# Optimization experiments

Measured on AMD Instinct MI355X. Metric: run time of the kernel, lower is better.

Reference implementation:

```python
import jax, jax.numpy as jnp
import numpy as np

N, E, G = 50000, 800000, 64
IN, HID, H, OUT = 128, 64, 4, 10


def _gat_layer(x, src, dst, W, a_src, a_dst, b):
    # x: [N, Fin]; W: [H*C, Fin]; a_src/a_dst: [H, C]; b: [H*C]
    n = x.shape[0]
    C = a_src.shape[1]
    h = (x @ W.T).reshape(n, H, C)                      # [N, H, C]
    e_src = jnp.einsum('nhc,hc->nh', h, a_src)          # [N, H]
    e_dst = jnp.einsum('nhc,hc->nh', h, a_dst)          # [N, H]
    logits = jax.nn.leaky_relu(e_src[src] + e_dst[dst], 0.2)  # [E', H]
    # segment softmax over destination node
    m = jax.ops.segment_max(logits, dst, num_segments=n)
    ex = jnp.exp(logits - m[dst])
    denom = jax.ops.segment_sum(ex, dst, num_segments=n)
    alpha = ex / (denom[dst] + 1e-16)                   # [E', H]
    msg = h[src] * alpha[:, :, None]                    # [E', H, C]
    out = jax.ops.segment_sum(msg, dst, num_segments=n) # [N, H, C]
    return out.reshape(n, H * C) + b


def setup_inputs() -> dict:
    key = jax.random.key(0)
    ks = jax.random.split(key, 20)
    x = jax.random.normal(ks[0], (N, IN), dtype=jnp.float32)
    edge_index = jax.random.randint(ks[1], (2, E), 0, N, dtype=jnp.int64)
    batch = jnp.sort(jax.random.randint(ks[2], (N,), 0, G, dtype=jnp.int64))

    def glorot(k, shape):
        fan = shape[-1]
        return jax.random.normal(k, shape, dtype=jnp.float32) / jnp.sqrt(jnp.float32(fan))

    ins = [IN, HID * H, HID * H]
    params = {}
    for i, fin in enumerate(ins, start=1):
        params[f'W{i}'] = glorot(ks[3 * i], (H * HID, fin))
        params[f'a_src{i}'] = glorot(ks[3 * i + 1], (H, HID))
        params[f'a_dst{i}'] = glorot(ks[3 * i + 2], (H, HID))
        params[f'b{i}'] = jnp.zeros((H * HID,), dtype=jnp.float32)
    params['Wl'] = glorot(ks[13], (OUT, H * HID))
    params['bl'] = jnp.zeros((OUT,), dtype=jnp.float32)
    return dict(x=x, edge_index=edge_index, batch=batch, **params)


def reference(x, edge_index, batch,
              W1, a_src1, a_dst1, b1,
              W2, a_src2, a_dst2, b2,
              W3, a_src3, a_dst3, b3,
              Wl, bl):
    n = x.shape[0]
    loops = jnp.arange(n, dtype=edge_index.dtype)
    src = jnp.concatenate([edge_index[0], loops])  # add self-loops (PyG default)
    dst = jnp.concatenate([edge_index[1], loops])

    h = jax.nn.elu(_gat_layer(x, src, dst, W1, a_src1, a_dst1, b1))
    h = jax.nn.elu(_gat_layer(h, src, dst, W2, a_src2, a_dst2, b2))
    h = _gat_layer(h, src, dst, W3, a_src3, a_dst3, b3)

    # global mean pool over graphs
    sums = jax.ops.segment_sum(h, batch, num_segments=G)          # [G, H*HID]
    counts = jax.ops.segment_sum(jnp.ones((n,), h.dtype), batch, num_segments=G)
    pooled = sums / jnp.maximum(counts, 1.0)[:, None]
    return pooled @ Wl.T + bl                                      # [G, OUT]
```

## Files before the change

kernel.cpp:

```cpp
#include <hip/hip_runtime.h>
#include <hip/hip_bf16.h>
#include <math.h>

#define NNODES 50000
#define NEDGES 800000
#define NGRAPH 64
#define FIN 128
#define HC 256
#define NHEAD 4
#define NOUT 10
#define ETOT (NEDGES + NNODES)
#define NB196 ((NNODES + 255) / 256)
#define BUCKET_MAX 5376
#define S1CHUNK 4096
#define NBS1 ((ETOT + S1CHUNK - 1) / S1CHUNK)


typedef unsigned short u16;
typedef unsigned char u8;
typedef __attribute__((ext_vector_type(8))) short short8;
typedef __attribute__((ext_vector_type(4))) float f32x4;
typedef __attribute__((ext_vector_type(2))) float f32x2;

__device__ inline u16 f2b(float f) {
    union { float f; unsigned u; } v; v.f = f;
    unsigned r = v.u + 0x7FFF + ((v.u >> 16) & 1);
    return (u16)(r >> 16);
}
__device__ inline float b2f(u16 u) {
    union { unsigned u; float f; } v; v.u = ((unsigned)u) << 16; return v.f;
}

__device__ inline void gload_lds16(const void* g, void* l) {
    __builtin_amdgcn_global_load_lds(
        (const __attribute__((address_space(1))) unsigned*)g,
        (__attribute__((address_space(3))) unsigned*)l, 16, 0, 0);
}


#define CS0 (NNODES * FIN)
#define CS1 (HC * FIN)
#define CS2 (HC * HC)
#define NBCONV (((CS0 + CS1 + 2 * CS2) / 4 + 255) / 256)
#define NBDEG ((ETOT + 255) / 256)

__global__ void prep_kernel(const float* __restrict__ x, const float* __restrict__ W1,
                            const float* __restrict__ W2, const float* __restrict__ W3,
                            u16* __restrict__ xb, u16* __restrict__ w1b,
                            u16* __restrict__ w2b, u16* __restrict__ w3b,
                            const int* __restrict__ ei, int* __restrict__ deg) {
    int b = blockIdx.x;
    if (b < NBCONV) {
        long i = (long)(b * 256 + threadIdx.x) * 4;
        if (i < CS0) {
            float4 v = *(const float4*)(x + i);
            ushort4 o;
            o.x = f2b(v.x); o.y = f2b(v.y); o.z = f2b(v.z); o.w = f2b(v.w);
            *(ushort4*)(xb + i) = o;
        } else if (i < CS0 + CS1) {
            long off = i - CS0;
            float4 v = *(const float4*)(W1 + off);
            ushort4 o;
            o.x = f2b(v.x); o.y = f2b(v.y); o.z = f2b(v.z); o.w = f2b(v.w);
            *(ushort4*)(w1b + off) = o;
        } else if (i < CS0 + CS1 + 2 * CS2) {
            const float* src; u16* dst; long off;
            if (i < CS0 + CS1 + CS2) { src = W2; dst = w2b; off = i - CS0 - CS1; }
            else                     { src = W3; dst = w3b; off = i - CS0 - CS1 - CS2; }
            float4 v = *(const float4*)(src + off);
            int row = (int)(off >> 8), col = (int)(off & 255);
            float vv[4] = {v.x, v.y, v.z, v.w};
            #pragma unroll
            for (int k = 0; k < 4; ++k) {
                int c = col + k;
                int pp = (c & ~63) | ((c & 15) << 2) | ((c >> 4) & 3);
                dst[row * 256 + pp] = f2b(vv[k]);
            }
        }
    } else {
        int e = (b - NBCONV) * 256 + threadIdx.x;
        if (e >= ETOT) return;
        int dstn = (e < NEDGES) ? ei[NEDGES + e] : (e - NEDGES);
        atomicAdd(&deg[dstn], 1);
    }
}


__global__ __launch_bounds__(256) void scan1_kernel(const int* __restrict__ deg,
                                                    int* __restrict__ off,
                                                    int* __restrict__ bsum) {
    int tid = threadIdx.x, lane = tid & 63, wid = tid >> 6;
    int i = blockIdx.x * 256 + tid;
    __shared__ int ws[4];
    int v = (i < NNODES) ? deg[i] : 0;
    int x = v;
    #pragma unroll
    for (int o = 1; o < 64; o <<= 1) {
        int t = __shfl_up(x, o);
        if (lane >= o) x += t;
    }
    if (lane == 63) ws[wid] = x;
    __syncthreads();
    if (tid < 4) {
        int w = ws[tid];
        #pragma unroll
        for (int o = 1; o < 4; o <<= 1) {
            int t = __shfl_up(w, o, 4);
            if ((tid & 3) >= o) w += t;
        }
        ws[tid] = w;
    }
    __syncthreads();
    int wexcl = wid ? ws[wid - 1] : 0;
    if (i <= NNODES) off[i] = x - v + wexcl;
    if (tid == 0) bsum[blockIdx.x] = ws[3];
}

__global__ __launch_bounds__(256) void scan2_kernel(int* __restrict__ bsum,
                                                    const int* __restrict__ batch,
                                                    int* __restrict__ goff) {
    int tid = threadIdx.x, lane = tid & 63, wid = tid >> 6;
    __shared__ int ws[4];
    int v = (tid < NB196) ? bsum[tid] : 0;
    int x = v;
    #pragma unroll
    for (int o = 1; o < 64; o <<= 1) {
        int t = __shfl_up(x, o);
        if (lane >= o) x += t;
    }
    if (lane == 63) ws[wid] = x;
    __syncthreads();
    if (tid < 4) {
        int w = ws[tid];
        #pragma unroll
        for (int o = 1; o < 4; o <<= 1) {
            int t = __shfl_up(w, o, 4);
            if ((tid & 3) >= o) w += t;
        }
        ws[tid] = w;
    }
    __syncthreads();
    int wexcl = wid ? ws[wid - 1] : 0;
    if (tid <= NB196) bsum[tid] = x - v + wexcl;
    if (tid <= NGRAPH) {
        int g = tid, lo = 0, hi = NNODES;
        while (lo < hi) {
            int mid = (lo + hi) >> 1;
            if (batch[mid] < g) lo = mid + 1; else hi = mid;
        }
        goff[g] = lo;
    }
}


__global__ __launch_bounds__(256) void scatter1_kernel(const int* __restrict__ ei,
                                                       const int* __restrict__ bsum,
                                                       int* __restrict__ bcur,
                                                       unsigned* __restrict__ tmp) {
    __shared__ int hist[NB196];
    __shared__ int basec[NB196];
    int tid = threadIdx.x;
    int e0 = blockIdx.x * S1CHUNK;
    for (int i = tid; i < NB196; i += 256) hist[i] = 0;
    __syncthreads();
    int bkt[16], rnk[16];
    unsigned pk[16];
    #pragma unroll
    for (int k = 0; k < 16; ++k) {
        int e = e0 + k * 256 + tid;
        bkt[k] = -1;
        if (e < ETOT) {
            int src, dst;
            if (e < NEDGES) { src = ei[e]; dst = ei[NEDGES + e]; }
            else            { src = dst = e - NEDGES; }
            int b = dst >> 8;
            bkt[k] = b;
            rnk[k] = atomicAdd(&hist[b], 1);
            pk[k] = (unsigned)src | ((unsigned)(dst & 255) << 16);
        }
    }
    __syncthreads();
    for (int i = tid; i < NB196; i += 256) {
        int h = hist[i];
        basec[i] = h ? atomicAdd(&bcur[i], h) : 0;
    }
    __syncthreads();
    #pragma unroll
    for (int k = 0; k < 16; ++k) {
        if (bkt[k] >= 0)
            tmp[bsum[bkt[k]] + basec[bkt[k]] + rnk[k]] = pk[k];
    }
}

__global__ __launch_bounds__(256) void scatter2_kernel(const unsigned* __restrict__ tmp,
                                                       const int* __restrict__ off,
                                                       const int* __restrict__ bsum,
                                                       int* __restrict__ ssrc) {
    __shared__ int cnt[256];
    __shared__ int ldss[BUCKET_MAX];
    int b = blockIdx.x;
    int tid = threadIdx.x;
    int s = bsum[b], e2 = bsum[b + 1];
    int total = e2 - s;
    if (total > BUCKET_MAX) total = BUCKET_MAX;
    cnt[tid] = 0;
    __syncthreads();
    const int* offb = off + b * 256;
    for (int i = s + tid; i < e2; i += 256) {
        unsigned pk = tmp[i];
        int src = (int)(pk & 0xFFFFu);
        int ld = (int)(pk >> 16);
        int rank = atomicAdd(&cnt[ld], 1);
        int idx = offb[ld] + rank;
        if (idx < BUCKET_MAX) ldss[idx] = src;
    }
    __syncthreads();
    for (int i = tid; i < total; i += 256)
        ssrc[s + i] = ldss[i];
}


#define TBM 128
#define TBN 128
#define TBK 32

__global__ __launch_bounds__(256) void gemm_mfma(const u16* __restrict__ A,
                                                 const u16* __restrict__ B,
                                                 u8* __restrict__ C, int K,
                                                 const float* __restrict__ asrc,
                                                 const float* __restrict__ adst,
                                                 float* __restrict__ es,
                                                 float* __restrict__ ed) {
    __shared__ u16 Als[TBM * TBK];
    __shared__ u16 Bls[TBN * TBK];
    int tid = threadIdx.x;
    int wave = tid >> 6, lane = tid & 63;
    int brow = blockIdx.x * TBM, bcol = blockIdx.y * TBN;
    int m_base = (wave >> 1) * 64, n_base = (wave & 1) * 64;
    int r0 = tid >> 2, kc = (tid & 3) * 8;
    int lquad = lane >> 4, l16 = lane & 15;

    f32x4 acc[4][4] = {};

    const u16* ga0 = A + (size_t)(brow + r0) * K + kc;
    const u16* ga1 = A + (size_t)(brow + 64 + r0) * K + kc;
    const u16* gb0 = B + (size_t)(bcol + r0) * K + kc;
    const u16* gb1 = B + (size_t)(bcol + 64 + r0) * K + kc;
    u16* la0 = &Als[r0 * TBK + kc];
    u16* la1 = &Als[(64 + r0) * TBK + kc];
    u16* lb0 = &Bls[r0 * TBK + kc];
    u16* lb1 = &Bls[(64 + r0) * TBK + kc];

    for (int k0 = 0; k0 < K; k0 += TBK) {
        __syncthreads();
        gload_lds16(ga0 + k0, la0);
        gload_lds16(ga1 + k0, la1);
        gload_lds16(gb0 + k0, lb0);
        gload_lds16(gb1 + k0, lb1);
        __syncthreads();
        short8 fa[4], fb[4];
        #pragma unroll
        for (int i = 0; i < 4; ++i) {
            fa[i] = *(const short8*)(&Als[(m_base + i * 16 + l16) * TBK + lquad * 8]);
            fb[i] = *(const short8*)(&Bls[(n_base + i * 16 + l16) * TBK + lquad * 8]);
        }
        #pragma unroll
        for (int i = 0; i < 4; ++i)
            #pragma unroll
            for (int j = 0; j < 4; ++j)
                acc[i][j] = __builtin_amdgcn_mfma_f32_16x16x32_bf16(fa[i], fb[j], acc[i][j], 0, 0, 0);
    }

    #pragma unroll
    for (int i = 0; i < 4; ++i) {
        int rbase = brow + m_base + i * 16 + lquad * 4;
        #pragma unroll
        for (int r = 0; r < 4; ++r) {
            int row = rbase + r;
            if (row < NNODES) {
                int u = 0;
                u = __builtin_amdgcn_cvt_pk_fp8_f32(acc[i][0][r], acc[i][1][r], u, false);
                u = __builtin_amdgcn_cvt_pk_fp8_f32(acc[i][2][r], acc[i][3][r], u, true);
                *(int*)(C + (size_t)row * HC + bcol + n_base + l16 * 4) = u;
            }
        }
    }

    int head = (bcol + n_base) >> 6;
    float asv[4], adv[4];
    #pragma unroll
    for (int j = 0; j < 4; ++j) {
        asv[j] = asrc[head * 64 + j * 16 + l16];
        adv[j] = adst[head * 64 + j * 16 + l16];
    }
    #pragma unroll
    for (int i = 0; i < 4; ++i) {
        #pragma unroll
        for (int r = 0; r < 4; ++r) {
            float ps = 0.f, pd = 0.f;
            #pragma unroll
            for (int j = 0; j < 4; ++j) {
                ps = fmaf(acc[i][j][r], asv[j], ps);
                pd = fmaf(acc[i][j][r], adv[j], pd);
            }
            #pragma unroll
            for (int o = 1; o < 16; o <<= 1) {
                ps += __shfl_xor(ps, o);
                pd += __shfl_xor(pd, o);
            }
            int row = brow + m_base + i * 16 + lquad * 4 + r;
            if (l16 == 0 && row < NNODES) {
                es[row * 4 + head] = ps;
                ed[row * 4 + head] = pd;
            }
        }
    }
}


__global__ __launch_bounds__(256) void aggregate_kernel(const u8* __restrict__ h,
                                                        const int* __restrict__ ssrc,
                                                        const int* __restrict__ off,
                                                        const int* __restrict__ bsum,
                                                        const float* __restrict__ es,
                                                        const float* __restrict__ ed,
                                                        const float* __restrict__ bias,
                                                        u16* __restrict__ out,
                                                        int apply_elu) {
    __shared__ int2 xch[4][4][17];
    const unsigned* h32 = (const unsigned*)h;
    int wid = threadIdx.x >> 6;
    int dst = blockIdx.x * 4 + wid;
    if (dst >= NNODES) return;
    int lane = threadIdx.x & 63;
    int head = lane >> 4;
    int j16 = lane & 15;
    int s = off[dst] + bsum[dst >> 8];
    int e = off[dst + 1] + bsum[(dst + 1) >> 8];
    float edh = ed[dst * 4 + head];
    int2* myslot = &xch[wid][head][0];

    float a0 = 0.f, a1 = 0.f, a2 = 0.f, a3 = 0.f, dpriv = 0.f;

    int base = s;
    for (; base + 16 <= e; base += 16) {
        int mysrc = ssrc[base + j16];
        float l = es[mysrc * 4 + head] + edh;
        l = fmaxf(l, 0.2f * l);
        float myex = __expf(l);
        dpriv += myex;
        myslot[j16] = make_int2(mysrc, __float_as_int(myex));
        #pragma unroll
        for (int j = 0; j < 16; ++j) {
            int2 pr = myslot[j];
            float exj = __int_as_float(pr.y);
            unsigned hv = h32[(unsigned)pr.x * 64 + lane];
            f32x2 lo = __builtin_amdgcn_cvt_pk_f32_fp8(hv, false);
            f32x2 hi = __builtin_amdgcn_cvt_pk_f32_fp8(hv, true);
            a0 += lo.x * exj;
            a1 += lo.y * exj;
            a2 += hi.x * exj;
            a3 += hi.y * exj;
        }
    }
    int cnt = e - base;
    if (cnt > 0) {
        int mysrc = 0; float myex = 0.f;
        if (j16 < cnt) {
            mysrc = ssrc[base + j16];
            float l = es[mysrc * 4 + head] + edh;
            l = fmaxf(l, 0.2f * l);
            myex = __expf(l);
            dpriv += myex;
        }
        myslot[j16] = make_int2(mysrc, __float_as_int(myex));
        for (int j = 0; j < cnt; ++j) {
            int2 pr = myslot[j];
            float exj = __int_as_float(pr.y);
            unsigned hv = h32[(unsigned)pr.x * 64 + lane];
            f32x2 lo = __builtin_amdgcn_cvt_pk_f32_fp8(hv, false);
            f32x2 hi = __builtin_amdgcn_cvt_pk_f32_fp8(hv, true);
            a0 += lo.x * exj;
            a1 += lo.y * exj;
            a2 += hi.x * exj;
            a3 += hi.y * exj;
        }
    }
    #pragma unroll
    for (int o = 1; o < 16; o <<= 1) dpriv += __shfl_xor(dpriv, o);
    float inv = 1.f / (dpriv + 1e-16f);
    int bbase = ((lane >> 4) << 6) | (lane & 15);
    float b0 = bias[bbase], b1 = bias[bbase + 16], b2 = bias[bbase + 32], b3 = bias[bbase + 48];
    float o0 = a0 * inv + b0;
    float o1 = a1 * inv + b1;
    float o2 = a2 * inv + b2;
    float o3 = a3 * inv + b3;
    if (apply_elu) {
        o0 = o0 > 0.f ? o0 : __expf(o0) - 1.f;
        o1 = o1 > 0.f ? o1 : __expf(o1) - 1.f;
        o2 = o2 > 0.f ? o2 : __expf(o2) - 1.f;
        o3 = o3 > 0.f ? o3 : __expf(o3) - 1.f;
    }
    ushort4 ov;
    ov.x = f2b(o0); ov.y = f2b(o1); ov.z = f2b(o2); ov.w = f2b(o3);
    *(ushort4*)(out + (size_t)dst * HC + lane * 4) = ov;
}


__global__ __launch_bounds__(256) void pool_kernel(const u16* __restrict__ hin,
                                                   const int* __restrict__ goff,
                                                   float* __restrict__ pp) {
    int g = blockIdx.x;
    int slice = blockIdx.y;
    int lane = threadIdx.x & 63;
    int wid = threadIdx.x >> 6;
    int s = goff[g], e = goff[g + 1];
    float a0 = 0.f, a1 = 0.f, a2 = 0.f, a3 = 0.f;
    for (int n = s + slice * 4 + wid; n < e; n += 32) {
        ushort4 hv = *(const ushort4*)(hin + (size_t)n * HC + lane * 4);
        a0 += b2f(hv.x); a1 += b2f(hv.y); a2 += b2f(hv.z); a3 += b2f(hv.w);
    }
    __shared__ float4 part[4][64];
    part[wid][lane] = make_float4(a0, a1, a2, a3);
    __syncthreads();
    if (wid == 0) {
        float4 p0 = part[0][lane], p1 = part[1][lane], p2 = part[2][lane], p3 = part[3][lane];
        float4 v = make_float4((p0.x + p1.x) + (p2.x + p3.x),
                               (p0.y + p1.y) + (p2.y + p3.y),
                               (p0.z + p1.z) + (p2.z + p3.z),
                               (p0.w + p1.w) + (p2.w + p3.w));
        *(float4*)(pp + ((size_t)(g * 8 + slice)) * HC + lane * 4) = v;
    }
}


__global__ __launch_bounds__(64) void final_kernel(const float* __restrict__ pp,
                                                   const int* __restrict__ goff,
                                                   const float* __restrict__ Wl,
                                                   const float* __restrict__ bl,
                                                   float* __restrict__ out) {
    int g = blockIdx.x;
    int lane = threadIdx.x;
    float4 pv = make_float4(0.f, 0.f, 0.f, 0.f);
    #pragma unroll
    for (int sl = 0; sl < 8; ++sl) {
        float4 v = *(const float4*)(pp + ((size_t)(g * 8 + sl)) * HC + lane * 4);
        pv.x += v.x; pv.y += v.y; pv.z += v.z; pv.w += v.w;
    }
    float cntf = fmaxf((float)(goff[g + 1] - goff[g]), 1.f);
    float inv = 1.f / cntf;
    pv.x *= inv; pv.y *= inv; pv.z *= inv; pv.w *= inv;
    int wbase = ((lane >> 4) << 6) | (lane & 15);
    float acc[NOUT];
    #pragma unroll
    for (int o = 0; o < NOUT; ++o) {
        const float* w = Wl + o * HC + wbase;
        acc[o] = pv.x * w[0] + pv.y * w[16] + pv.z * w[32] + pv.w * w[48];
    }
    #pragma unroll
    for (int s = 32; s > 0; s >>= 1)
        #pragma unroll
        for (int o = 0; o < NOUT; ++o)
            acc[o] += __shfl_xor(acc[o], s);
    if (lane == 0) {
        #pragma unroll
        for (int o = 0; o < NOUT; ++o)
            out[g * NOUT + o] = acc[o] + bl[o];
    }
}


extern "C" void kernel_launch(void* const* d_in, const int* in_sizes, int n_in,
                              void* d_out, int out_size, void* d_ws, size_t ws_size,
                              hipStream_t stream) {
    (void)in_sizes; (void)n_in; (void)out_size; (void)ws_size;
    const float* x   = (const float*)d_in[0];
    const int*   ei  = (const int*)d_in[1];
    const int*   bat = (const int*)d_in[2];
    const float* W1  = (const float*)d_in[3];
    const float* as1 = (const float*)d_in[4];
    const float* ad1 = (const float*)d_in[5];
    const float* b1  = (const float*)d_in[6];
    const float* W2  = (const float*)d_in[7];
    const float* as2 = (const float*)d_in[8];
    const float* ad2 = (const float*)d_in[9];
    const float* b2  = (const float*)d_in[10];
    const float* W3  = (const float*)d_in[11];
    const float* as3 = (const float*)d_in[12];
    const float* ad3 = (const float*)d_in[13];
    const float* b3  = (const float*)d_in[14];
    const float* Wl  = (const float*)d_in[15];
    const float* bl  = (const float*)d_in[16];
    float* out = (float*)d_out;

    char* ws = (char*)d_ws;
    size_t p = 0;
    auto alloc = [&](size_t bytes) {
        size_t a = p;
        p += (bytes + 255) & ~(size_t)255;
        return a;
    };
    int*      off  = (int*)(ws + alloc((NNODES + 1) * 4));
    int*      deg  = (int*)(ws + alloc((size_t)NNODES * 4));
    int*      bcur = (int*)(ws + alloc(256 * 4));
    int*      ssrc = (int*)(ws + alloc((size_t)ETOT * 4));
    unsigned* tmp  = (unsigned*)(ws + alloc((size_t)ETOT * 4));
    int*      bsum = (int*)(ws + alloc(256 * 4));
    float*    es   = (float*)(ws + alloc((size_t)NNODES * NHEAD * 4));
    float*    ed   = (float*)(ws + alloc((size_t)NNODES * NHEAD * 4));
    u16*      xb   = (u16*)(ws + alloc((size_t)NNODES * FIN * 2));
    u16*      w1b  = (u16*)(ws + alloc((size_t)HC * FIN * 2));
    u16*      w2b  = (u16*)(ws + alloc((size_t)HC * HC * 2));
    u16*      w3b  = (u16*)(ws + alloc((size_t)HC * HC * 2));
    u8*       Hb   = (u8*)(ws + alloc((size_t)NNODES * HC));
    u16*      Ab   = (u16*)(ws + alloc((size_t)NNODES * HC * 2));
    float*    pp   = (float*)(ws + alloc((size_t)NGRAPH * 8 * HC * 4));
    int*      goff = (int*)(ws + alloc((size_t)(NGRAPH + 1) * 4));
    alloc(128 * 1024);

    hipMemsetAsync(deg, 0, (size_t)((char*)ssrc - (char*)deg), stream);

    prep_kernel<<<NBCONV + NBDEG, 256, 0, stream>>>(x, W1, W2, W3, xb, w1b, w2b, w3b, ei, deg);

    scan1_kernel<<<NB196, 256, 0, stream>>>(deg, off, bsum);
    scan2_kernel<<<1, 256, 0, stream>>>(bsum, bat, goff);
    scatter1_kernel<<<NBS1, 256, 0, stream>>>(ei, bsum, bcur, tmp);
    scatter2_kernel<<<NB196, 256, 0, stream>>>(tmp, off, bsum, ssrc);

    dim3 ggrid((NNODES + TBM - 1) / TBM, HC / TBN);
    int nblocks4 = (NNODES + 3) / 4;

    gemm_mfma<<<ggrid, 256, 0, stream>>>(xb, w1b, Hb, FIN, as1, ad1, es, ed);
    aggregate_kernel<<<nblocks4, 256, 0, stream>>>(Hb, ssrc, off, bsum, es, ed, b1, Ab, 1);
    gemm_mfma<<<ggrid, 256, 0, stream>>>(Ab, w2b, Hb, HC, as2, ad2, es, ed);
    aggregate_kernel<<<nblocks4, 256, 0, stream>>>(Hb, ssrc, off, bsum, es, ed, b2, Ab, 1);
    gemm_mfma<<<ggrid, 256, 0, stream>>>(Ab, w3b, Hb, HC, as3, ad3, es, ed);
    aggregate_kernel<<<nblocks4, 256, 0, stream>>>(Hb, ssrc, off, bsum, es, ed, b3, Ab, 0);

    dim3 pgrid(NGRAPH, 8);
    pool_kernel<<<pgrid, 256, 0, stream>>>(Ab, goff, pp);
    final_kernel<<<NGRAPH, 64, 0, stream>>>(pp, goff, Wl, bl, out);
}
```

Measured before the change: 372.5 us.

## Build CSR via fixed-capacity buckets and widen aggregate gathers to 16-byte loads

Replaces the degree-atomic, two-scan, two-scatter CSR build with a single bucket scatter into fixed-capacity per-bucket slots. This is followed by a small bucket scan and a per-bucket local counting sort that also writes the per-node offsets. It drops the global degree atomics, one kernel launch and a memset of a large buffer. Separately, the aggregate kernel now has each 16-lane group gather a different edge's full 256-byte fp8 row with 128-bit loads and combines the groups by cross-lane shuffle reduction. This cuts the number of gather instructions but adds 16 accumulators per lane and extra shuffles. Any bucket holding more than its fixed capacity is silently truncated.

```diff
diff --git a/kernel.cpp b/kernel.cpp
--- a/kernel.cpp
+++ b/kernel.cpp
@@ -11,7 +11,7 @@
 #define NOUT 10
 #define ETOT (NEDGES + NNODES)
 #define NB196 ((NNODES + 255) / 256)
-#define BUCKET_MAX 5376
+#define BCAP 5376
 #define S1CHUNK 4096
 #define NBS1 ((ETOT + S1CHUNK - 1) / S1CHUNK)
 
@@ -21,6 +21,7 @@
 typedef __attribute__((ext_vector_type(8))) short short8;
 typedef __attribute__((ext_vector_type(4))) float f32x4;
 typedef __attribute__((ext_vector_type(2))) float f32x2;
+typedef __attribute__((ext_vector_type(4))) unsigned uint4v;
 
 __device__ inline u16 f2b(float f) {
     union { float f; unsigned u; } v; v.f = f;
@@ -42,86 +43,91 @@
 #define CS1 (HC * FIN)
 #define CS2 (HC * HC)
 #define NBCONV (((CS0 + CS1 + 2 * CS2) / 4 + 255) / 256)
-#define NBDEG ((ETOT + 255) / 256)
 
 __global__ void prep_kernel(const float* __restrict__ x, const float* __restrict__ W1,
                             const float* __restrict__ W2, const float* __restrict__ W3,
                             u16* __restrict__ xb, u16* __restrict__ w1b,
-                            u16* __restrict__ w2b, u16* __restrict__ w3b,
-                            const int* __restrict__ ei, int* __restrict__ deg) {
+                            u16* __restrict__ w2b, u16* __restrict__ w3b) {
     int b = blockIdx.x;
-    if (b < NBCONV) {
-        long i = (long)(b * 256 + threadIdx.x) * 4;
-        if (i < CS0) {
-            float4 v = *(const float4*)(x + i);
-            ushort4 o;
-            o.x = f2b(v.x); o.y = f2b(v.y); o.z = f2b(v.z); o.w = f2b(v.w);
-            *(ushort4*)(xb + i) = o;
-        } else if (i < CS0 + CS1) {
-            long off = i - CS0;
-            float4 v = *(const float4*)(W1 + off);
-            ushort4 o;
-            o.x = f2b(v.x); o.y = f2b(v.y); o.z = f2b(v.z); o.w = f2b(v.w);
-            *(ushort4*)(w1b + off) = o;
-        } else if (i < CS0 + CS1 + 2 * CS2) {
-            const float* src; u16* dst; long off;
-            if (i < CS0 + CS1 + CS2) { src = W2; dst = w2b; off = i - CS0 - CS1; }
-            else                     { src = W3; dst = w3b; off = i - CS0 - CS1 - CS2; }
-            float4 v = *(const float4*)(src + off);
-            int row = (int)(off >> 8), col = (int)(off & 255);
-            float vv[4] = {v.x, v.y, v.z, v.w};
-            #pragma unroll
-            for (int k = 0; k < 4; ++k) {
-                int c = col + k;
-                int pp = (c & ~63) | ((c & 15) << 2) | ((c >> 4) & 3);
-                dst[row * 256 + pp] = f2b(vv[k]);
-            }
-        }
-    } else {
-        int e = (b - NBCONV) * 256 + threadIdx.x;
-        if (e >= ETOT) return;
-        int dstn = (e < NEDGES) ? ei[NEDGES + e] : (e - NEDGES);
-        atomicAdd(&deg[dstn], 1);
-    }
-}
-
-
-__global__ __launch_bounds__(256) void scan1_kernel(const int* __restrict__ deg,
-                                                    int* __restrict__ off,
-                                                    int* __restrict__ bsum) {
-    int tid = threadIdx.x, lane = tid & 63, wid = tid >> 6;
-    int i = blockIdx.x * 256 + tid;
-    __shared__ int ws[4];
-    int v = (i < NNODES) ? deg[i] : 0;
-    int x = v;
-    #pragma unroll
-    for (int o = 1; o < 64; o <<= 1) {
-        int t = __shfl_up(x, o);
-        if (lane >= o) x += t;
-    }
-    if (lane == 63) ws[wid] = x;
-    __syncthreads();
-    if (tid < 4) {
-        int w = ws[tid];
-        #pragma unroll
-        for (int o = 1; o < 4; o <<= 1) {
-            int t = __shfl_up(w, o, 4);
-            if ((tid & 3) >= o) w += t;
-        }
-        ws[tid] = w;
-    }
-    __syncthreads();
-    int wexcl = wid ? ws[wid - 1] : 0;
-    if (i <= NNODES) off[i] = x - v + wexcl;
-    if (tid == 0) bsum[blockIdx.x] = ws[3];
-}
-
-__global__ __launch_bounds__(256) void scan2_kernel(int* __restrict__ bsum,
+    long i = (long)(b * 256 + threadIdx.x) * 4;
+    if (i < CS0) {
+        float4 v = *(const float4*)(x + i);
+        ushort4 o;
+        o.x = f2b(v.x); o.y = f2b(v.y); o.z = f2b(v.z); o.w = f2b(v.w);
+        *(ushort4*)(xb + i) = o;
+    } else if (i < CS0 + CS1) {
+        long off = i - CS0;
+        float4 v = *(const float4*)(W1 + off);
+        ushort4 o;
+        o.x = f2b(v.x); o.y = f2b(v.y); o.z = f2b(v.z); o.w = f2b(v.w);
+        *(ushort4*)(w1b + off) = o;
+    } else if (i < CS0 + CS1 + 2 * CS2) {
+        const float* src; u16* dst; long off;
+        if (i < CS0 + CS1 + CS2) { src = W2; dst = w2b; off = i - CS0 - CS1; }
+        else                     { src = W3; dst = w3b; off = i - CS0 - CS1 - CS2; }
+        float4 v = *(const float4*)(src + off);
+        int row = (int)(off >> 8), col = (int)(off & 255);
+        float vv[4] = {v.x, v.y, v.z, v.w};
+        #pragma unroll
+        for (int k = 0; k < 4; ++k) {
+            int c = col + k;
+            int pp = (c & ~63) | ((c & 15) << 2) | ((c >> 4) & 3);
+            dst[row * 256 + pp] = f2b(vv[k]);
+        }
+    }
+}
+
+
+__global__ __launch_bounds__(256) void scatter1_kernel(const int* __restrict__ ei,
+                                                       int* __restrict__ bcur,
+                                                       unsigned* __restrict__ tmp) {
+    __shared__ int hist[NB196];
+    __shared__ int basec[NB196];
+    int tid = threadIdx.x;
+    int e0 = blockIdx.x * S1CHUNK;
+    for (int i = tid; i < NB196; i += 256) hist[i] = 0;
+    __syncthreads();
+    int bkt[16], rnk[16];
+    unsigned pk[16];
+    #pragma unroll
+    for (int k = 0; k < 16; ++k) {
+        int e = e0 + k * 256 + tid;
+        bkt[k] = -1;
+        if (e < ETOT) {
+            int src, dstn;
+            if (e < NEDGES) { src = ei[e]; dstn = ei[NEDGES + e]; }
+            else            { src = dstn = e - NEDGES; }
+            int b = dstn >> 8;
+            bkt[k] = b;
+            rnk[k] = atomicAdd(&hist[b], 1);
+            pk[k] = (unsigned)src | ((unsigned)(dstn & 255) << 16);
+        }
+    }
+    __syncthreads();
+    for (int i = tid; i < NB196; i += 256) {
+        int h = hist[i];
+        basec[i] = h ? atomicAdd(&bcur[i], h) : 0;
+    }
+    __syncthreads();
+    #pragma unroll
+    for (int k = 0; k < 16; ++k) {
+        if (bkt[k] >= 0) {
+            int pos = basec[bkt[k]] + rnk[k];
+            if (pos < BCAP)
+                tmp[(size_t)bkt[k] * BCAP + pos] = pk[k];
+        }
+    }
+}
+
+
+__global__ __launch_bounds__(256) void scanb_kernel(const int* __restrict__ bcur,
+                                                    int* __restrict__ bsum,
                                                     const int* __restrict__ batch,
                                                     int* __restrict__ goff) {
     int tid = threadIdx.x, lane = tid & 63, wid = tid >> 6;
     __shared__ int ws[4];
-    int v = (tid < NB196) ? bsum[tid] : 0;
+    int v = 0;
+    if (tid < NB196) { v = bcur[tid]; if (v > BCAP) v = BCAP; }
     int x = v;
     #pragma unroll
     for (int o = 1; o < 64; o <<= 1) {
@@ -153,70 +159,61 @@
 }
 
 
-__global__ __launch_bounds__(256) void scatter1_kernel(const int* __restrict__ ei,
+__global__ __launch_bounds__(256) void scatter2_kernel(const unsigned* __restrict__ tmp,
+                                                       const int* __restrict__ bcur,
                                                        const int* __restrict__ bsum,
-                                                       int* __restrict__ bcur,
-                                                       unsigned* __restrict__ tmp) {
-    __shared__ int hist[NB196];
-    __shared__ int basec[NB196];
-    int tid = threadIdx.x;
-    int e0 = blockIdx.x * S1CHUNK;
-    for (int i = tid; i < NB196; i += 256) hist[i] = 0;
-    __syncthreads();
-    int bkt[16], rnk[16];
-    unsigned pk[16];
-    #pragma unroll
-    for (int k = 0; k < 16; ++k) {
-        int e = e0 + k * 256 + tid;
-        bkt[k] = -1;
-        if (e < ETOT) {
-            int src, dst;
-            if (e < NEDGES) { src = ei[e]; dst = ei[NEDGES + e]; }
-            else            { src = dst = e - NEDGES; }
-            int b = dst >> 8;
-            bkt[k] = b;
-            rnk[k] = atomicAdd(&hist[b], 1);
-            pk[k] = (unsigned)src | ((unsigned)(dst & 255) << 16);
-        }
-    }
-    __syncthreads();
-    for (int i = tid; i < NB196; i += 256) {
-        int h = hist[i];
-        basec[i] = h ? atomicAdd(&bcur[i], h) : 0;
-    }
-    __syncthreads();
-    #pragma unroll
-    for (int k = 0; k < 16; ++k) {
-        if (bkt[k] >= 0)
-            tmp[bsum[bkt[k]] + basec[bkt[k]] + rnk[k]] = pk[k];
-    }
-}
-
-__global__ __launch_bounds__(256) void scatter2_kernel(const unsigned* __restrict__ tmp,
-                                                       const int* __restrict__ off,
-                                                       const int* __restrict__ bsum,
+                                                       int* __restrict__ off,
                                                        int* __restrict__ ssrc) {
+    __shared__ unsigned ebuf[BCAP];
+    __shared__ int ldss[BCAP];
     __shared__ int cnt[256];
-    __shared__ int ldss[BUCKET_MAX];
+    __shared__ int loff[256];
+    __shared__ int ws[4];
     int b = blockIdx.x;
     int tid = threadIdx.x;
-    int s = bsum[b], e2 = bsum[b + 1];
-    int total = e2 - s;
-    if (total > BUCKET_MAX) total = BUCKET_MAX;
+    int n = bcur[b];
+    if (n > BCAP) n = BCAP;
     cnt[tid] = 0;
-    __syncthreads();
-    const int* offb = off + b * 256;
-    for (int i = s + tid; i < e2; i += 256) {
-        unsigned pk = tmp[i];
-        int src = (int)(pk & 0xFFFFu);
+    const unsigned* tb = tmp + (size_t)b * BCAP;
+    for (int i = tid; i < n; i += 256) ebuf[i] = tb[i];
+    __syncthreads();
+    for (int i = tid; i < n; i += 256) atomicAdd(&cnt[ebuf[i] >> 16], 1);
+    __syncthreads();
+    int lane = tid & 63, wid = tid >> 6;
+    int v = cnt[tid];
+    int x = v;
+    #pragma unroll
+    for (int o = 1; o < 64; o <<= 1) {
+        int t = __shfl_up(x, o);
+        if (lane >= o) x += t;
+    }
+    if (lane == 63) ws[wid] = x;
+    __syncthreads();
+    if (tid < 4) {
+        int w = ws[tid];
+        #pragma unroll
+        for (int o = 1; o < 4; o <<= 1) {
+            int t = __shfl_up(w, o, 4);
+            if ((tid & 3) >= o) w += t;
+        }
+        ws[tid] = w;
+    }
+    __syncthreads();
+    int wexcl = wid ? ws[wid - 1] : 0;
+    int excl = x - v + wexcl;
+    loff[tid] = excl;
+    off[b * 256 + tid] = excl;
+    cnt[tid] = 0;
+    __syncthreads();
+    for (int i = tid; i < n; i += 256) {
+        unsigned pk = ebuf[i];
         int ld = (int)(pk >> 16);
         int rank = atomicAdd(&cnt[ld], 1);
-        int idx = offb[ld] + rank;
-        if (idx < BUCKET_MAX) ldss[idx] = src;
-    }
-    __syncthreads();
-    for (int i = tid; i < total; i += 256)
-        ssrc[s + i] = ldss[i];
+        ldss[loff[ld] + rank] = (int)(pk & 0xFFFFu);
+    }
+    __syncthreads();
+    int s = bsum[b];
+    for (int i = tid; i < n; i += 256) ssrc[s + i] = ldss[i];
 }
 
 
@@ -328,73 +325,85 @@
                                                         u16* __restrict__ out,
                                                         int apply_elu) {
     __shared__ int2 xch[4][4][17];
-    const unsigned* h32 = (const unsigned*)h;
+    const uint4v* h128 = (const uint4v*)h;
     int wid = threadIdx.x >> 6;
     int dst = blockIdx.x * 4 + wid;
     if (dst >= NNODES) return;
     int lane = threadIdx.x & 63;
-    int head = lane >> 4;
+    int headp = lane >> 4;
     int j16 = lane & 15;
+    int g = lane >> 4;
+    int q = lane & 15;
+    int headc = q >> 2;
     int s = off[dst] + bsum[dst >> 8];
     int e = off[dst + 1] + bsum[(dst + 1) >> 8];
-    float edh = ed[dst * 4 + head];
-    int2* myslot = &xch[wid][head][0];
-
-    float a0 = 0.f, a1 = 0.f, a2 = 0.f, a3 = 0.f, dpriv = 0.f;
-
-    int base = s;
-    for (; base + 16 <= e; base += 16) {
-        int mysrc = ssrc[base + j16];
-        float l = es[mysrc * 4 + head] + edh;
-        l = fmaxf(l, 0.2f * l);
-        float myex = __expf(l);
-        dpriv += myex;
-        myslot[j16] = make_int2(mysrc, __float_as_int(myex));
-        #pragma unroll
-        for (int j = 0; j < 16; ++j) {
-            int2 pr = myslot[j];
-            float exj = __int_as_float(pr.y);
-            unsigned hv = h32[(unsigned)pr.x * 64 + lane];
-            f32x2 lo = __builtin_amdgcn_cvt_pk_f32_fp8(hv, false);
-            f32x2 hi = __builtin_amdgcn_cvt_pk_f32_fp8(hv, true);
-            a0 += lo.x * exj;
-            a1 += lo.y * exj;
-            a2 += hi.x * exj;
-            a3 += hi.y * exj;
-        }
-    }
-    int cnt = e - base;
-    if (cnt > 0) {
-        int mysrc = 0; float myex = 0.f;
+    float edh = ed[dst * 4 + headp];
+    int2* pslot = &xch[wid][headp][0];
+    const int2* cslot = &xch[wid][headc][0];
+
+    float acc[16] = {};
+    float dpriv = 0.f;
+
+    for (int base = s; base < e; base += 16) {
+        int cnt = e - base;
+        if (cnt > 16) cnt = 16;
+        int mysrc = 0;
+        float myex = 0.f;
         if (j16 < cnt) {
             mysrc = ssrc[base + j16];
-            float l = es[mysrc * 4 + head] + edh;
+            float l = es[mysrc * 4 + headp] + edh;
             l = fmaxf(l, 0.2f * l);
             myex = __expf(l);
             dpriv += myex;
         }
-        myslot[j16] = make_int2(mysrc, __float_as_int(myex));
-        for (int j = 0; j < cnt; ++j) {
-            int2 pr = myslot[j];
+        pslot[j16] = make_int2(mysrc, __float_as_int(myex));
+        #pragma unroll
+        for (int j = 0; j < 4; ++j) {
+            if (j * 4 >= cnt) break;
+            int2 pr = cslot[j * 4 + g];
             float exj = __int_as_float(pr.y);
-            unsigned hv = h32[(unsigned)pr.x * 64 + lane];
-            f32x2 lo = __builtin_amdgcn_cvt_pk_f32_fp8(hv, false);
-            f32x2 hi = __builtin_amdgcn_cvt_pk_f32_fp8(hv, true);
-            a0 += lo.x * exj;
-            a1 += lo.y * exj;
-            a2 += hi.x * exj;
-            a3 += hi.y * exj;
-        }
-    }
+            uint4v hv = h128[(((unsigned)pr.x) << 4) + (unsigned)q];
+            #pragma unroll
+            for (int u = 0; u < 4; ++u) {
+                f32x2 lo = __builtin_amdgcn_cvt_pk_f32_fp8(hv[u], false);
+                f32x2 hi = __builtin_amdgcn_cvt_pk_f32_fp8(hv[u], true);
+                acc[u * 4 + 0] += lo.x * exj;
+                acc[u * 4 + 1] += lo.y * exj;
+                acc[u * 4 + 2] += hi.x * exj;
+                acc[u * 4 + 3] += hi.y * exj;
+            }
+        }
+    }
+
     #pragma unroll
     for (int o = 1; o < 16; o <<= 1) dpriv += __shfl_xor(dpriv, o);
     float inv = 1.f / (dpriv + 1e-16f);
-    int bbase = ((lane >> 4) << 6) | (lane & 15);
-    float b0 = bias[bbase], b1 = bias[bbase + 16], b2 = bias[bbase + 32], b3 = bias[bbase + 48];
-    float o0 = a0 * inv + b0;
-    float o1 = a1 * inv + b1;
-    float o2 = a2 * inv + b2;
-    float o3 = a3 * inv + b3;
+    float invc = __shfl(inv, headc << 4);
+
+    #pragma unroll
+    for (int k = 0; k < 8; ++k) {
+        float snd = (lane & 32) ? acc[k] : acc[k + 8];
+        float rcv = __shfl_xor(snd, 32);
+        if (lane & 32) acc[k + 8] += rcv; else acc[k] += rcv;
+    }
+    #pragma unroll
+    for (int k = 0; k < 8; ++k)
+        if (lane & 32) acc[k] = acc[k + 8];
+    #pragma unroll
+    for (int k = 0; k < 4; ++k) {
+        float snd = (lane & 16) ? acc[k] : acc[k + 4];
+        float rcv = __shfl_xor(snd, 16);
+        if (lane & 16) acc[k + 4] += rcv; else acc[k] += rcv;
+    }
+    #pragma unroll
+    for (int k = 0; k < 4; ++k)
+        if (lane & 16) acc[k] = acc[k + 4];
+
+    int cbase = headc * 64 + (q & 3) * 4 + g;
+    float o0 = acc[0] * invc + bias[cbase];
+    float o1 = acc[1] * invc + bias[cbase + 16];
+    float o2 = acc[2] * invc + bias[cbase + 32];
+    float o3 = acc[3] * invc + bias[cbase + 48];
     if (apply_elu) {
         o0 = o0 > 0.f ? o0 : __expf(o0) - 1.f;
         o1 = o1 > 0.f ? o1 : __expf(o1) - 1.f;
@@ -403,7 +412,7 @@
     }
     ushort4 ov;
     ov.x = f2b(o0); ov.y = f2b(o1); ov.z = f2b(o2); ov.w = f2b(o3);
-    *(ushort4*)(out + (size_t)dst * HC + lane * 4) = ov;
+    *(ushort4*)(out + (size_t)dst * HC + q * 16 + g * 4) = ov;
 }
 
 
@@ -500,11 +509,10 @@
         p += (bytes + 255) & ~(size_t)255;
         return a;
     };
-    int*      off  = (int*)(ws + alloc((NNODES + 1) * 4));
-    int*      deg  = (int*)(ws + alloc((size_t)NNODES * 4));
+    int*      off  = (int*)(ws + alloc((size_t)(NB196 * 256 + 256) * 4));
     int*      bcur = (int*)(ws + alloc(256 * 4));
     int*      ssrc = (int*)(ws + alloc((size_t)ETOT * 4));
-    unsigned* tmp  = (unsigned*)(ws + alloc((size_t)ETOT * 4));
+    unsigned* tmp  = (unsigned*)(ws + alloc((size_t)NB196 * BCAP * 4));
     int*      bsum = (int*)(ws + alloc(256 * 4));
     float*    es   = (float*)(ws + alloc((size_t)NNODES * NHEAD * 4));
     float*    ed   = (float*)(ws + alloc((size_t)NNODES * NHEAD * 4));
@@ -518,14 +526,13 @@
     int*      goff = (int*)(ws + alloc((size_t)(NGRAPH + 1) * 4));
     alloc(128 * 1024);
 
-    hipMemsetAsync(deg, 0, (size_t)((char*)ssrc - (char*)deg), stream);
-
-    prep_kernel<<<NBCONV + NBDEG, 256, 0, stream>>>(x, W1, W2, W3, xb, w1b, w2b, w3b, ei, deg);
-
-    scan1_kernel<<<NB196, 256, 0, stream>>>(deg, off, bsum);
-    scan2_kernel<<<1, 256, 0, stream>>>(bsum, bat, goff);
-    scatter1_kernel<<<NBS1, 256, 0, stream>>>(ei, bsum, bcur, tmp);
-    scatter2_kernel<<<NB196, 256, 0, stream>>>(tmp, off, bsum, ssrc);
+    hipMemsetAsync(bcur, 0, 256 * 4, stream);
+
+    prep_kernel<<<NBCONV, 256, 0, stream>>>(x, W1, W2, W3, xb, w1b, w2b, w3b);
+
+    scatter1_kernel<<<NBS1, 256, 0, stream>>>(ei, bcur, tmp);
+    scanb_kernel<<<1, 256, 0, stream>>>(bcur, bsum, bat, goff);
+    scatter2_kernel<<<NB196, 256, 0, stream>>>(tmp, bcur, bsum, off, ssrc);
 
     dim3 ggrid((NNODES + TBM - 1) / TBM, HC / TBN);
     int nblocks4 = (NNODES + 3) / 4;
```

Measured after the change: 356.9 us. 4.2% less time.
